# Performance work log

Measured on AMD Instinct MI355X. Metric: run time of the kernel, lower is better.

Reference implementation:

```python
import jax, jax.numpy as jnp
import numpy as np

B, N, M = 8, 131072, 64
M_VALID = 48  # trailing padding, matches remove_pad semantics
POSITIVE_IOU = 0.5
NEGATIVE_IOU = 0.3
CLASS_NUM = 1  # hardcoded in RpnTarget.__init__


def _make_boxes(key, shape_prefix, max_wh=64.0, span=1024.0):
    k1, k2, k3, k4 = jax.random.split(key, 4)
    x1 = jax.random.uniform(k1, shape_prefix, minval=0.0, maxval=span)
    y1 = jax.random.uniform(k2, shape_prefix, minval=0.0, maxval=span)
    w = jax.random.uniform(k3, shape_prefix, minval=4.0, maxval=max_wh)
    h = jax.random.uniform(k4, shape_prefix, minval=4.0, maxval=max_wh)
    return jnp.stack([x1, y1, x1 + w, y1 + h], axis=-1)


def setup_inputs() -> dict:
    key = jax.random.key(0)
    ka, kb = jax.random.split(key, 2)
    prior_anchors = _make_boxes(ka, (B, N))                       # [B,N,4]
    boxes = _make_boxes(kb, (B, M), max_wh=128.0)                 # [B,M,4]
    status = jnp.concatenate(
        [jnp.ones((B, M_VALID, 1)), jnp.zeros((B, M - M_VALID, 1))], axis=1
    )
    gt_bboxes = jnp.concatenate([boxes, status], axis=-1)          # [B,M,5]
    gt_class_idxes = jnp.zeros((B, M, 2), dtype=jnp.int32)         # zeroed in call()
    return {
        "prior_anchors": prior_anchors,
        "gt_bboxes": gt_bboxes,
        "gt_class_idxes": gt_class_idxes,
    }


def _bbox_transform(anchors, bboxes):
    # anchors, bboxes: [..., 4] in [x1,y1,x2,y2]
    ax = (anchors[..., 0] + anchors[..., 2]) * 0.5
    ay = (anchors[..., 1] + anchors[..., 3]) * 0.5
    aw = anchors[..., 2] - anchors[..., 0]
    ah = anchors[..., 3] - anchors[..., 1]
    bx = (bboxes[..., 0] + bboxes[..., 2]) * 0.5
    by = (bboxes[..., 1] + bboxes[..., 3]) * 0.5
    bw = bboxes[..., 2] - bboxes[..., 0]
    bh = bboxes[..., 3] - bboxes[..., 1]
    tx = (bx - ax) / aw
    ty = (by - ay) / ah
    tw = jnp.log(bw / aw)
    th = jnp.log(bh / ah)
    return jnp.stack([tx, ty, tw, th], axis=-1)


def _rpn_targets(prior_anchors, gt_bboxes, gt_class_idxes):
    boxes = gt_bboxes[..., :4]                 # [B,M,4]
    valid = gt_bboxes[..., 4] > 0              # [B,M] padding status

    a = prior_anchors[:, :, None, :]           # [B,N,1,4]
    b = boxes[:, None, :, :]                   # [B,1,M,4]
    inter_w = jnp.maximum(jnp.minimum(a[..., 2], b[..., 2]) - jnp.maximum(a[..., 0], b[..., 0]), 0.0)
    inter_h = jnp.maximum(jnp.minimum(a[..., 3], b[..., 3]) - jnp.maximum(a[..., 1], b[..., 1]), 0.0)
    inter = inter_w * inter_h                  # [B,N,M]
    area_a = jnp.maximum(a[..., 2] - a[..., 0], 0.0) * jnp.maximum(a[..., 3] - a[..., 1], 0.0)
    area_b = jnp.maximum(b[..., 2] - b[..., 0], 0.0) * jnp.maximum(b[..., 3] - b[..., 1], 0.0)
    iou = inter / (area_a + area_b - inter)    # [B,N,M]
    # mask out padded gt boxes (equivalent to remove_pad + trailing padding)
    iou = jnp.where(valid[:, None, :], iou, -1.0)

    max_iou = jnp.max(iou, axis=-1)            # [B,N]
    match_idx = jnp.argmax(iou, axis=-1)       # [B,N]
    positive = max_iou >= POSITIVE_IOU
    ignore = (max_iou >= NEGATIVE_IOU) & ~positive

    matched_boxes = jnp.take_along_axis(boxes, match_idx[..., None], axis=1)  # [B,N,4]
    reg = _bbox_transform(prior_anchors, matched_boxes)                        # [B,N,4]

    status = jnp.where(positive, 1.0, jnp.where(ignore, -1.0, 0.0))[..., None]  # [B,N,1]

    # call() zeros gt_class_idxes, so matched class idx is always 0; one_hot depth 1 -> ones
    cls_idx = jnp.take_along_axis(
        jnp.zeros_like(gt_class_idxes)[..., 0], match_idx, axis=1
    )                                                                           # [B,N] int32 zeros
    cls = jax.nn.one_hot(cls_idx, CLASS_NUM, dtype=reg.dtype)                   # [B,N,1]

    regression_targets = jnp.concatenate([reg, status], axis=-1)                # [B,N,5]
    classification_targets = jnp.concatenate([cls, status], axis=-1)            # [B,N,2]
    return regression_targets, classification_targets


def reference(prior_anchors, gt_bboxes, gt_class_idxes):
    return _rpn_targets(prior_anchors, gt_bboxes, gt_class_idxes)
```

## Files before the change

kernel.cpp:

```cpp
#include <hip/hip_runtime.h>


#define BB    8
#define NN    131072
#define MM    64
#define BLK   256
#define NBLK  (NN / BLK)
#define GC    16
#define CELLS (GC * GC)
#define CAP   32

#define WS_BOXES 0
#define WS_AREA  8192
#define WS_CNT   10240
#define WS_LIST  10272
#define WS_LEN   75808

__global__ __launch_bounds__(256) void rpn_build_lists(
    const float* __restrict__ gt, char* __restrict__ ws)
{
    __shared__ float4 sbox[MM];
    __shared__ int    scnt;

    const int b = blockIdx.x;
    const int t = threadIdx.x;

    float4* wboxes = (float4*)(ws + WS_BOXES);
    float*  warea  = (float*)(ws + WS_AREA);
    int*    wcnt   = (int*)(ws + WS_CNT);
    unsigned char* wlist = (unsigned char*)(ws + WS_LIST);
    unsigned char* wlen  = (unsigned char*)(ws + WS_LEN);

    if (t < MM) {
        const float* g = gt + ((size_t)b * MM + t) * 5;
        float x1 = g[0], y1 = g[1], x2 = g[2], y2 = g[3], st = g[4];
        bool valid = (st > 0.0f);
        unsigned long long mask = __ballot(valid);
        int slot = __popcll(mask & ((1ull << t) - 1ull));
        if (t == 0) { scnt = __popcll(mask); wcnt[b] = __popcll(mask); }
        if (valid) {
            float4 bx = make_float4(x1, y1, x2, y2);
            sbox[slot] = bx;
            wboxes[b * MM + slot] = bx;
            warea[b * MM + slot]  = fmaxf(x2 - x1, 0.0f) * fmaxf(y2 - y1, 0.0f);
        }
    }
    __syncthreads();

    const int cnt = scnt;
    const int cx = t & (GC - 1), cy = t >> 4;
    const float wx1 = cx * 64.0f, wx2 = wx1 + 128.0f;
    const float wy1 = cy * 64.0f, wy2 = wy1 + 128.0f;

    int len = 0;
    for (int s = 0; s < cnt; ++s) {
        float4 bx = sbox[s];
        if (bx.x <= wx2 && bx.z >= wx1 && bx.y <= wy2 && bx.w >= wy1) {
            if (len < CAP)
                wlist[(size_t)b * CELLS * CAP + (size_t)len * CELLS + t]
                    = (unsigned char)s;
            ++len;
        }
    }
    wlen[(size_t)b * CELLS + t] = (unsigned char)len;
}

__global__ __launch_bounds__(BLK) void rpn_target_kernel(
    const float* __restrict__ anchors,
    const float* __restrict__ gt,
    const char* __restrict__ ws,
    float* __restrict__ out)
{
    constexpr float INV = GC / 1024.0f;

    __shared__ float sx1[MM], sy1[MM], sx2[MM], sy2[MM], sar[MM];
    __shared__ uint4 slist4[CELLS * CAP / 16];
    __shared__ uint  slen32[CELLS / 4];
    __shared__ int   scnt;

    const int t = threadIdx.x;
    const int b = blockIdx.x / NBLK;
    const int n = (blockIdx.x % NBLK) * BLK + t;

    if (t < MM) {
        float4 bx = ((const float4*)(ws + WS_BOXES))[b * MM + t];
        sx1[t] = bx.x; sy1[t] = bx.y; sx2[t] = bx.z; sy2[t] = bx.w;
        sar[t] = ((const float*)(ws + WS_AREA))[b * MM + t];
    }
    if (t == 0) scnt = ((const int*)(ws + WS_CNT))[b];
    if (t < CELLS / 4)
        slen32[t] = ((const uint*)(ws + WS_LEN + (size_t)b * CELLS))[t];
    {
        const uint4* src = (const uint4*)(ws + WS_LIST + (size_t)b * CELLS * CAP);
        slist4[t * 2]     = src[t * 2];
        slist4[t * 2 + 1] = src[t * 2 + 1];
    }
    __syncthreads();

    const unsigned char* slist = (const unsigned char*)slist4;
    const unsigned char* slen  = (const unsigned char*)slen32;

    const float4 a = ((const float4*)anchors)[(size_t)b * NN + n];
    const float area_a = fmaxf(a.z - a.x, 0.0f) * fmaxf(a.w - a.y, 0.0f);
    const int cnt = scnt;

    int cx = (int)(a.x * INV); cx = cx < 0 ? 0 : (cx > GC - 1 ? GC - 1 : cx);
    int cy = (int)(a.y * INV); cy = cy < 0 ? 0 : (cy > GC - 1 ? GC - 1 : cy);
    const int cid = cy * GC + cx;

    const int len   = slen[cid];
    const bool full = (len > CAP);
    const int mylen = full ? cnt : len;

    float best  = 0.0f;
    int   bslot = 0;
    for (int j = 0; ; ++j) {
        if (!__any(j < mylen)) break;
        if (j < mylen) {
            const int idx = full ? j : (int)slist[j * CELLS + cid];
            const float bx1 = sx1[idx], by1 = sy1[idx];
            const float bx2 = sx2[idx], by2 = sy2[idx];
            const float ab  = sar[idx];
            float iw = fmaxf(fminf(a.z, bx2) - fmaxf(a.x, bx1), 0.0f);
            float ih = fmaxf(fminf(a.w, by2) - fmaxf(a.y, by1), 0.0f);
            float inter = iw * ih;
            if (inter > 0.0f) {
                float denom = (area_a + ab) - inter;
                float iou = inter / denom;
                if (iou > best) { best = iou; bslot = idx; }
            }
        }
    }

    const bool positive = (best >= 0.5f);
    const bool ignore   = (best >= 0.3f) && !positive;
    const float status  = positive ? 1.0f : (ignore ? -1.0f : 0.0f);

    float mx1, my1, mx2, my2;
    if (cnt > 0) {
        mx1 = sx1[bslot]; my1 = sy1[bslot]; mx2 = sx2[bslot]; my2 = sy2[bslot];
    } else {
        const float* g0 = gt + (size_t)b * MM * 5;
        mx1 = g0[0]; my1 = g0[1]; mx2 = g0[2]; my2 = g0[3];
    }

    const float aw  = a.z - a.x;
    const float ah  = a.w - a.y;
    const float rw  = __builtin_amdgcn_rcpf(aw);
    const float rh  = __builtin_amdgcn_rcpf(ah);
    const float axc = (a.x + a.z) * 0.5f;
    const float ayc = (a.y + a.w) * 0.5f;
    const float bxc = (mx1 + mx2) * 0.5f;
    const float byc = (my1 + my2) * 0.5f;
    const float bw  = mx2 - mx1;
    const float bh  = my2 - my1;
    const float tx  = (bxc - axc) * rw;
    const float ty  = (byc - ayc) * rh;
    const float LN2 = 0.69314718055994531f;
    const float tw  = __builtin_amdgcn_logf(bw * rw) * LN2;
    const float th  = __builtin_amdgcn_logf(bh * rh) * LN2;

    const size_t gid = (size_t)b * NN + n;

    float* r = out + gid * 5;
    r[0] = tx; r[1] = ty; r[2] = tw; r[3] = th; r[4] = status;

    float2* c = (float2*)(out + (size_t)BB * NN * 5) + gid;
    *c = make_float2(1.0f, status);
}

extern "C" void kernel_launch(void* const* d_in, const int* in_sizes, int n_in,
                              void* d_out, int out_size, void* d_ws, size_t ws_size,
                              hipStream_t stream) {
    const float* anchors = (const float*)d_in[0];
    const float* gt      = (const float*)d_in[1];

    float* out = (float*)d_out;
    char*  ws  = (char*)d_ws;

    hipLaunchKernelGGL(rpn_build_lists, dim3(BB), dim3(256), 0, stream, gt, ws);
    hipLaunchKernelGGL(rpn_target_kernel, dim3(BB * NBLK), dim3(BLK), 0, stream,
                       anchors, gt, ws, out);
}
```

Baseline: 25.41 us.

## Store per-cell candidate lists contiguously and read them directly from global memory

The list builder now writes each grid cell's candidate indices contiguously, pads unused entries with 0xFF, and zeroes the unused box slots. The target kernel drops the per-block shared-memory staging of all cell lists and lengths. Each thread instead loads its own cell's first eight indices as one 64-bit word and evaluates them branch-free in an unrolled loop. Longer lists and the overflow case fall back to slower paths. This removes the per-block copy of about 8 KB of lists into shared memory, issues the anchor load before the barrier, and trades divergent loops for fixed work on eight padded slots.

```diff
diff --git a/kernel.cpp b/kernel.cpp
--- a/kernel.cpp
+++ b/kernel.cpp
@@ -37,13 +37,18 @@
         bool valid = (st > 0.0f);
         unsigned long long mask = __ballot(valid);
         int slot = __popcll(mask & ((1ull << t) - 1ull));
-        if (t == 0) { scnt = __popcll(mask); wcnt[b] = __popcll(mask); }
+        int cntL = __popcll(mask);
+        if (t == 0) { scnt = cntL; wcnt[b] = cntL; }
         if (valid) {
             float4 bx = make_float4(x1, y1, x2, y2);
             sbox[slot] = bx;
             wboxes[b * MM + slot] = bx;
             warea[b * MM + slot]  = fmaxf(x2 - x1, 0.0f) * fmaxf(y2 - y1, 0.0f);
         }
+        if (t >= cntL) {
+            wboxes[b * MM + t] = make_float4(0.f, 0.f, 0.f, 0.f);
+            warea[b * MM + t]  = 0.f;
+        }
     }
     __syncthreads();
 
@@ -52,13 +57,16 @@
     const float wx1 = cx * 64.0f, wx2 = wx1 + 128.0f;
     const float wy1 = cy * 64.0f, wy2 = wy1 + 128.0f;
 
+    unsigned long long* lq =
+        (unsigned long long*)(wlist + ((size_t)b * CELLS + t) * CAP);
+    lq[0] = ~0ull; lq[1] = ~0ull; lq[2] = ~0ull; lq[3] = ~0ull;
+    unsigned char* lst = (unsigned char*)lq;
+
     int len = 0;
     for (int s = 0; s < cnt; ++s) {
         float4 bx = sbox[s];
         if (bx.x <= wx2 && bx.z >= wx1 && bx.y <= wy2 && bx.w >= wy1) {
-            if (len < CAP)
-                wlist[(size_t)b * CELLS * CAP + (size_t)len * CELLS + t]
-                    = (unsigned char)s;
+            if (len < CAP) lst[len] = (unsigned char)s;
             ++len;
         }
     }
@@ -74,13 +82,13 @@
     constexpr float INV = GC / 1024.0f;
 
     __shared__ float sx1[MM], sy1[MM], sx2[MM], sy2[MM], sar[MM];
-    __shared__ uint4 slist4[CELLS * CAP / 16];
-    __shared__ uint  slen32[CELLS / 4];
     __shared__ int   scnt;
 
     const int t = threadIdx.x;
     const int b = blockIdx.x / NBLK;
     const int n = (blockIdx.x % NBLK) * BLK + t;
+
+    const float4 a = ((const float4*)anchors)[(size_t)b * NN + n];
 
     if (t < MM) {
         float4 bx = ((const float4*)(ws + WS_BOXES))[b * MM + t];
@@ -88,53 +96,75 @@
         sar[t] = ((const float*)(ws + WS_AREA))[b * MM + t];
     }
     if (t == 0) scnt = ((const int*)(ws + WS_CNT))[b];
-    if (t < CELLS / 4)
-        slen32[t] = ((const uint*)(ws + WS_LEN + (size_t)b * CELLS))[t];
-    {
-        const uint4* src = (const uint4*)(ws + WS_LIST + (size_t)b * CELLS * CAP);
-        slist4[t * 2]     = src[t * 2];
-        slist4[t * 2 + 1] = src[t * 2 + 1];
-    }
-    __syncthreads();
-
-    const unsigned char* slist = (const unsigned char*)slist4;
-    const unsigned char* slen  = (const unsigned char*)slen32;
-
-    const float4 a = ((const float4*)anchors)[(size_t)b * NN + n];
-    const float area_a = fmaxf(a.z - a.x, 0.0f) * fmaxf(a.w - a.y, 0.0f);
-    const int cnt = scnt;
 
     int cx = (int)(a.x * INV); cx = cx < 0 ? 0 : (cx > GC - 1 ? GC - 1 : cx);
     int cy = (int)(a.y * INV); cy = cy < 0 ? 0 : (cy > GC - 1 ? GC - 1 : cy);
     const int cid = cy * GC + cx;
 
-    const int len   = slen[cid];
-    const bool full = (len > CAP);
-    const int mylen = full ? cnt : len;
+    const unsigned long long lst8 = *(const unsigned long long*)
+        (ws + WS_LIST + ((size_t)b * CELLS + cid) * CAP);
+    const int len = ((const unsigned char*)(ws + WS_LEN))[(size_t)b * CELLS + cid];
+
+    const float area_a = fmaxf(a.z - a.x, 0.0f) * fmaxf(a.w - a.y, 0.0f);
+
+    __syncthreads();
+    const int cnt = scnt;
 
     float best  = 0.0f;
     int   bslot = 0;
-    for (int j = 0; ; ++j) {
-        if (!__any(j < mylen)) break;
-        if (j < mylen) {
-            const int idx = full ? j : (int)slist[j * CELLS + cid];
-            const float bx1 = sx1[idx], by1 = sy1[idx];
-            const float bx2 = sx2[idx], by2 = sy2[idx];
-            const float ab  = sar[idx];
-            float iw = fmaxf(fminf(a.z, bx2) - fmaxf(a.x, bx1), 0.0f);
-            float ih = fmaxf(fminf(a.w, by2) - fmaxf(a.y, by1), 0.0f);
+
+    float iou[8]; int id[8];
+    #pragma unroll
+    for (int j = 0; j < 8; ++j) {
+        const int raw = (int)((lst8 >> (8 * j)) & 0xFFull);
+        const int idx = raw & 63;
+        id[j] = idx;
+        const float bx1 = sx1[idx], by1 = sy1[idx];
+        const float bx2 = sx2[idx], by2 = sy2[idx];
+        float iw = fmaxf(fminf(a.z, bx2) - fmaxf(a.x, bx1), 0.0f);
+        float ih = fmaxf(fminf(a.w, by2) - fmaxf(a.y, by1), 0.0f);
+        float inter = iw * ih;
+        inter = (raw != 255) ? inter : 0.0f;
+        float denom = (area_a + sar[idx]) - inter;
+        iou[j] = inter / denom;
+    }
+    #pragma unroll
+    for (int j = 0; j < 8; ++j)
+        if (iou[j] > best) { best = iou[j]; bslot = id[j]; }
+
+    if (__any(len > 8)) {
+        const unsigned char* gl = (const unsigned char*)
+            (ws + WS_LIST + ((size_t)b * CELLS + cid) * CAP);
+        const int L = (len <= CAP) ? len : 0;
+        for (int j = 8; j < L; ++j) {
+            const int idx = gl[j];
+            float iw = fmaxf(fminf(a.z, sx2[idx]) - fmaxf(a.x, sx1[idx]), 0.0f);
+            float ih = fmaxf(fminf(a.w, sy2[idx]) - fmaxf(a.y, sy1[idx]), 0.0f);
             float inter = iw * ih;
             if (inter > 0.0f) {
-                float denom = (area_a + ab) - inter;
+                float denom = (area_a + sar[idx]) - inter;
                 float iou = inter / denom;
                 if (iou > best) { best = iou; bslot = idx; }
             }
         }
     }
-
-    const bool positive = (best >= 0.5f);
-    const bool ignore   = (best >= 0.3f) && !positive;
-    const float status  = positive ? 1.0f : (ignore ? -1.0f : 0.0f);
+    if (__any(len > CAP)) {
+        if (len > CAP) {
+            best = 0.0f; bslot = 0;
+            for (int j = 0; j < cnt; ++j) {
+                float iw = fmaxf(fminf(a.z, sx2[j]) - fmaxf(a.x, sx1[j]), 0.0f);
+                float ih = fmaxf(fminf(a.w, sy2[j]) - fmaxf(a.y, sy1[j]), 0.0f);
+                float inter = iw * ih;
+                if (inter > 0.0f) {
+                    float denom = (area_a + sar[j]) - inter;
+                    float iou = inter / denom;
+                    if (iou > best) { best = iou; bslot = j; }
+                }
+            }
+        }
+    }
+
+    const float status = (best >= 0.5f) ? 1.0f : ((best >= 0.3f) ? -1.0f : 0.0f);
 
     float mx1, my1, mx2, my2;
     if (cnt > 0) {
@@ -148,17 +178,11 @@
     const float ah  = a.w - a.y;
     const float rw  = __builtin_amdgcn_rcpf(aw);
     const float rh  = __builtin_amdgcn_rcpf(ah);
-    const float axc = (a.x + a.z) * 0.5f;
-    const float ayc = (a.y + a.w) * 0.5f;
-    const float bxc = (mx1 + mx2) * 0.5f;
-    const float byc = (my1 + my2) * 0.5f;
-    const float bw  = mx2 - mx1;
-    const float bh  = my2 - my1;
-    const float tx  = (bxc - axc) * rw;
-    const float ty  = (byc - ayc) * rh;
+    const float tx  = ((mx1 + mx2) * 0.5f - (a.x + a.z) * 0.5f) * rw;
+    const float ty  = ((my1 + my2) * 0.5f - (a.y + a.w) * 0.5f) * rh;
     const float LN2 = 0.69314718055994531f;
-    const float tw  = __builtin_amdgcn_logf(bw * rw) * LN2;
-    const float th  = __builtin_amdgcn_logf(bh * rh) * LN2;
+    const float tw  = __builtin_amdgcn_logf((mx2 - mx1) * rw) * LN2;
+    const float th  = __builtin_amdgcn_logf((my2 - my1) * rh) * LN2;
 
     const size_t gid = (size_t)b * NN + n;
 
```

Result: slower. 25.94 us (+2.1%).
